# Performance work log

Hardware: AMD Instinct MI355X
Metric: run time of the kernel (lower is better)

## Reference

```python
import jax, jax.numpy as jnp
import numpy as np

C = 512
GROUPS = 8
EPS = 1e-5


def setup_inputs() -> dict:
    key = jax.random.key(0)
    ks = jax.random.split(key, 7)
    b, c, h, w = 32, C, 32, 32
    x = jax.random.normal(ks[0], (b, c, h, w), dtype=jnp.float32)
    norm_gamma = jnp.ones((c,), dtype=jnp.float32)
    norm_beta = jnp.zeros((c,), dtype=jnp.float32)
    # 1x1 convs == per-pixel linear layers; store as [out, in] matrices
    qkv_w = jax.random.normal(ks[1], (3 * c, c), dtype=jnp.float32) * (1.0 / np.sqrt(c))
    qkv_b = jnp.zeros((3 * c,), dtype=jnp.float32)
    out_w = jax.random.normal(ks[2], (c, c), dtype=jnp.float32) * (1.0 / np.sqrt(c))
    out_b = jnp.zeros((c,), dtype=jnp.float32)
    return {"x": x, "norm_gamma": norm_gamma, "norm_beta": norm_beta,
            "qkv_w": qkv_w, "qkv_b": qkv_b, "out_w": out_w, "out_b": out_b}


def group_norm(x, gamma, beta):
    b, c, h, w = x.shape
    xg = x.reshape(b, GROUPS, c // GROUPS, h, w)
    mean = jnp.mean(xg, axis=(2, 3, 4), keepdims=True)
    var = jnp.var(xg, axis=(2, 3, 4), keepdims=True)
    xg = (xg - mean) * jax.lax.rsqrt(var + EPS)
    x = xg.reshape(b, c, h, w)
    return x * gamma[None, :, None, None] + beta[None, :, None, None]


def reference(x, norm_gamma, norm_beta, qkv_w, qkv_b, out_w, out_b):
    b, c, h, w = x.shape
    xn = group_norm(x, norm_gamma, norm_beta)
    # 1x1 conv: [b,c,h,w] -> [b,3c,h,w]
    qkv = jnp.einsum('oc,bchw->bohw', qkv_w, xn) + qkv_b[None, :, None, None]
    q, k, v = jnp.split(qkv.reshape(b, 3 * c, h * w), 3, axis=1)  # each [b,c,hw]
    scale = c ** (-0.5)
    attn = jnp.einsum('bci,bcj->bij', q, k) * scale  # [b, hw, hw]
    attn = jax.nn.softmax(attn, axis=-1)
    out = jnp.einsum('bij,bcj->bci', attn, v).reshape(b, c, h, w)
    out = jnp.einsum('oc,bchw->bohw', out_w, out) + out_b[None, :, None, None]
    return x + out
```

## Files before the change

kernel.cpp:

```cpp
#include <hip/hip_runtime.h>

#define HW 1024
#define CD 512

typedef __bf16 bf16x8 __attribute__((ext_vector_type(8)));
typedef float f32x4 __attribute__((ext_vector_type(4)));

__device__ __forceinline__ unsigned short f2bf(float f) {
    unsigned int u = __float_as_uint(f);
    u += 0x7fff + ((u >> 16) & 1);
    return (unsigned short)(u >> 16);
}
__device__ __forceinline__ float bf2f(unsigned short h) {
    return __uint_as_float((unsigned)h << 16);
}

#define AS1(p) ((__attribute__((address_space(1))) void*)(p))
#define AS3(p) ((__attribute__((address_space(3))) void*)(p))
#define GLD16(gp, lp) __builtin_amdgcn_global_load_lds(AS1(gp), AS3(lp), 16, 0, 0)

__global__ __launch_bounds__(256)
void gn_stats(const float* __restrict__ x, float* __restrict__ mean, float* __restrict__ rstd) {
    int bg = blockIdx.x;
    const float4* p4 = (const float4*)(x + (size_t)bg * 65536);
    int tid = threadIdx.x;
    float s = 0.f, ss = 0.f;
#pragma unroll 8
    for (int it = 0; it < 64; ++it) {
        float4 v = p4[tid + it * 256];
        s  += v.x + v.y + v.z + v.w;
        ss += v.x * v.x + v.y * v.y + v.z * v.z + v.w * v.w;
    }
#pragma unroll
    for (int d = 32; d > 0; d >>= 1) { s += __shfl_down(s, d); ss += __shfl_down(ss, d); }
    __shared__ float ls[4], lss[4];
    if ((tid & 63) == 0) { ls[tid >> 6] = s; lss[tid >> 6] = ss; }
    __syncthreads();
    if (tid == 0) {
        float S = ls[0] + ls[1] + ls[2] + ls[3];
        float SS = lss[0] + lss[1] + lss[2] + lss[3];
        float m = S * (1.f / 65536.f);
        float v = SS * (1.f / 65536.f) - m * m;
        mean[bg] = m;
        rstd[bg] = rsqrtf(v + 1e-5f);
    }
}

__global__ __launch_bounds__(256)
void gn_norm_t(const float* __restrict__ x, const float* __restrict__ mean, const float* __restrict__ rstd,
               const float* __restrict__ gamma, const float* __restrict__ beta,
               unsigned short* __restrict__ xnT) {
    __shared__ unsigned short tile[64][67];
    int i0 = blockIdx.x * 64, c0 = blockIdx.y * 64, b = blockIdx.z;
    float m = mean[b * 8 + blockIdx.y];
    float r = rstd[b * 8 + blockIdx.y];
    int tid = threadIdx.x;
    int tr = tid >> 4, tc = (tid & 15) * 4;
    const float* xb = x + ((size_t)b * CD + c0) * HW + i0;
#pragma unroll
    for (int p = 0; p < 4; ++p) {
        int c = tr + p * 16;
        float g = gamma[c0 + c] * r;
        float bb = beta[c0 + c] - m * g;
        float4 v = *(const float4*)(xb + (size_t)c * HW + tc);
        tile[c][tc + 0] = f2bf(v.x * g + bb);
        tile[c][tc + 1] = f2bf(v.y * g + bb);
        tile[c][tc + 2] = f2bf(v.z * g + bb);
        tile[c][tc + 3] = f2bf(v.w * g + bb);
    }
    __syncthreads();
    unsigned short* ob = xnT + ((size_t)b * HW + i0) * CD + c0;
#pragma unroll
    for (int p = 0; p < 4; ++p) {
        int ir = tr + p * 16;
        ushort4 u;
        u.x = tile[tc + 0][ir];
        u.y = tile[tc + 1][ir];
        u.z = tile[tc + 2][ir];
        u.w = tile[tc + 3][ir];
        *(ushort4*)(ob + (size_t)ir * CD + tc) = u;
    }
}

__global__ __launch_bounds__(256)
void tpose3_bf16(const float* __restrict__ qkv_w, unsigned short* __restrict__ dst0) {
    __shared__ unsigned short tile[64][67];
    const int zmap[3] = {0, 2, 1};
    const float* src = qkv_w + (size_t)blockIdx.z * CD * CD;
    unsigned short* dst = dst0 + (size_t)zmap[blockIdx.z] * CD * CD;
    int i0 = blockIdx.x * 64, c0 = blockIdx.y * 64;
    int tid = threadIdx.x;
    int tr = tid >> 4, tc = (tid & 15) * 4;
#pragma unroll
    for (int p = 0; p < 4; ++p) {
        int r = tr + p * 16;
        float4 v = *(const float4*)(src + (size_t)(i0 + r) * CD + c0 + tc);
        tile[r][tc + 0] = f2bf(v.x);
        tile[r][tc + 1] = f2bf(v.y);
        tile[r][tc + 2] = f2bf(v.z);
        tile[r][tc + 3] = f2bf(v.w);
    }
    __syncthreads();
#pragma unroll
    for (int p = 0; p < 4; ++p) {
        int ir = tr + p * 16;
        ushort4 u;
        u.x = tile[tc + 0][ir];
        u.y = tile[tc + 1][ir];
        u.z = tile[tc + 2][ir];
        u.w = tile[tc + 3][ir];
        *(ushort4*)(dst + (size_t)(c0 + ir) * CD + i0 + tc) = u;
    }
}

__global__ __launch_bounds__(256)
void cvt_bf16(const float* __restrict__ src, unsigned short* __restrict__ dst) {
    int i = blockIdx.x * 256 + threadIdx.x;
    float4 v = ((const float4*)src)[i];
    ushort4 u;
    u.x = f2bf(v.x); u.y = f2bf(v.y); u.z = f2bf(v.z); u.w = f2bf(v.w);
    ((ushort4*)dst)[i] = u;
}

__global__ __launch_bounds__(256)
void gvec_kernel(const float* __restrict__ wk, const float* __restrict__ bq,
                 float* __restrict__ g) {
    __shared__ float red[4][64];
    int d = blockIdx.x * 64 + (threadIdx.x & 63);
    int os = threadIdx.x >> 6;
    float acc = 0.f;
    for (int o = os * 128; o < os * 128 + 128; ++o)
        acc += wk[(size_t)o * CD + d] * bq[o];
    red[os][threadIdx.x & 63] = acc;
    __syncthreads();
    if (threadIdx.x < 64)
        g[blockIdx.x * 64 + threadIdx.x] = red[0][threadIdx.x] + red[1][threadIdx.x] +
                                           red[2][threadIdx.x] + red[3][threadIdx.x];
}

__global__ __launch_bounds__(256)
void bias2_kernel(const float* __restrict__ out_w, const float* __restrict__ bv,
                  float* __restrict__ bias2) {
    int wid = threadIdx.x >> 6, lane = threadIdx.x & 63;
    int o = blockIdx.x * 4 + wid;
    float acc = 0.f;
#pragma unroll
    for (int t = 0; t < 512; t += 64)
        acc += out_w[(size_t)o * CD + t + lane] * bv[t + lane];
#pragma unroll
    for (int d = 32; d > 0; d >>= 1) acc += __shfl_down(acc, d);
    if (lane == 0) bias2[o] = acc;
}

template<int EPI>
__global__ __launch_bounds__(256, 2)
void gemm_bt(const unsigned short* __restrict__ A, const unsigned short* __restrict__ B,
             void* __restrict__ Cv, const float* __restrict__ bias,
             int M, int N, int K, long long sA, long long sB, long long sC) {
    unsigned nx = gridDim.x, ny = gridDim.y;
    unsigned lin = blockIdx.x + nx * (blockIdx.y + ny * blockIdx.z);
    unsigned nwg = nx * ny * gridDim.z;
    unsigned work = (lin & 7) * (nwg >> 3) + (lin >> 3);
    unsigned bx = work % nx; work /= nx;
    unsigned by = work % ny;
    unsigned bz = work / ny;

    A += (size_t)bz * sA;
    B += (size_t)bz * sB;
    int m0 = by * 128, n0 = bx * 128;

    __shared__ unsigned short lA[2][128 * 64];
    __shared__ unsigned short lB[2][128 * 64];

    int tid = threadIdx.x;
    int lane = tid & 63;
    int wr = (tid >> 6) >> 1, wc = (tid >> 6) & 1;

    f32x4 acc[4][4] = {};

    int strow[4], stcol[4];
#pragma unroll
    for (int s = 0; s < 4; ++s) {
        int row = (s * 256 + tid) >> 3;
        int g = (tid & 7) ^ (row & 7);
        strow[s] = row;
        stcol[s] = g * 8;
    }

    auto stage = [&](int buf, int k0) {
#pragma unroll
        for (int s = 0; s < 4; ++s) {
            GLD16(A + (size_t)(m0 + strow[s]) * K + k0 + stcol[s], &lA[buf][(size_t)(s * 256 + tid) * 8]);
            GLD16(B + (size_t)(n0 + strow[s]) * K + k0 + stcol[s], &lB[buf][(size_t)(s * 256 + tid) * 8]);
        }
    };

    int NT = K >> 6;
    stage(0, 0);
    __syncthreads();
    int cur = 0;
    for (int t = 0; t < NT; ++t) {
        if (t + 1 < NT) stage(cur ^ 1, (t + 1) << 6);
        const char* pa = (const char*)lA[cur];
        const char* pb = (const char*)lB[cur];
#pragma unroll
        for (int kk = 0; kk < 64; kk += 32) {
            bf16x8 af[4], bfr[4];
#pragma unroll
            for (int m = 0; m < 4; ++m) {
                int row = wr * 64 + m * 16 + (lane & 15);
                int off = (row * 128 + (kk + (lane >> 4) * 8) * 2) ^ ((row & 7) << 4);
                af[m] = *(const bf16x8*)(pa + off);
            }
#pragma unroll
            for (int n = 0; n < 4; ++n) {
                int row = wc * 64 + n * 16 + (lane & 15);
                int off = (row * 128 + (kk + (lane >> 4) * 8) * 2) ^ ((row & 7) << 4);
                bfr[n] = *(const bf16x8*)(pb + off);
            }
#pragma unroll
            for (int m = 0; m < 4; ++m)
#pragma unroll
                for (int n = 0; n < 4; ++n)
                    acc[m][n] = __builtin_amdgcn_mfma_f32_16x16x32_bf16(af[m], bfr[n], acc[m][n], 0, 0, 0);
        }
        __syncthreads();
        cur ^= 1;
    }

    int rl = (lane >> 4) * 4;
    int cl = lane & 15;
    unsigned short* Cb = (unsigned short*)Cv + (size_t)bz * sC;
#pragma unroll
    for (int m = 0; m < 4; ++m)
#pragma unroll
        for (int n = 0; n < 4; ++n) {
            int gm = m0 + wr * 64 + m * 16 + rl;
            int gn = n0 + wc * 64 + n * 16 + cl;
#pragma unroll
            for (int rg = 0; rg < 4; ++rg) {
                float v = acc[m][n][rg];
                if (EPI == 0) v += bias[gn];
                if (EPI == 1) v += bias[gm + rg];
                Cb[(size_t)(gm + rg) * N + gn] = f2bf(v);
            }
        }
}

__global__ __launch_bounds__(256, 2)
void scores_gemm(const unsigned short* __restrict__ T1, const unsigned short* __restrict__ xnT,
                 unsigned short* __restrict__ S, float* __restrict__ tmax, float* __restrict__ tsum) {
    unsigned nx = gridDim.x, ny = gridDim.y;
    unsigned lin = blockIdx.x + nx * (blockIdx.y + ny * blockIdx.z);
    unsigned nwg = nx * ny * gridDim.z;
    unsigned work = (lin & 7) * (nwg >> 3) + (lin >> 3);
    unsigned bx = work % nx; work /= nx;
    unsigned by = work % ny;
    unsigned bz = work / ny;

    const unsigned short* Ab = T1 + (size_t)bz * HW * CD;
    const unsigned short* Bb = xnT + (size_t)bz * HW * CD;
    int m0 = by * 128, n0 = bx * 128;

    __shared__ unsigned short lA[2][128 * 64];
    __shared__ unsigned short lB[2][128 * 64];
    __shared__ float redm[2][128];
    __shared__ float reds[2][128];

    int tid = threadIdx.x, lane = tid & 63;
    int wr = (tid >> 6) >> 1, wc = (tid >> 6) & 1;

    f32x4 acc[4][4] = {};
    int strow[4], stcol[4];
#pragma unroll
    for (int s = 0; s < 4; ++s) {
        int row = (s * 256 + tid) >> 3;
        int g = (tid & 7) ^ (row & 7);
        strow[s] = row;
        stcol[s] = g * 8;
    }

    auto stage = [&](int buf, int k0) {
#pragma unroll
        for (int s = 0; s < 4; ++s) {
            GLD16(Ab + (size_t)(m0 + strow[s]) * CD + k0 + stcol[s], &lA[buf][(size_t)(s * 256 + tid) * 8]);
            GLD16(Bb + (size_t)(n0 + strow[s]) * CD + k0 + stcol[s], &lB[buf][(size_t)(s * 256 + tid) * 8]);
        }
    };

    stage(0, 0);
    __syncthreads();
    int cur = 0;
    for (int t = 0; t < 8; ++t) {
        if (t < 7) stage(cur ^ 1, (t + 1) << 6);
        const char* pa = (const char*)lA[cur];
        const char* pb = (const char*)lB[cur];
#pragma unroll
        for (int kk = 0; kk < 64; kk += 32) {
            bf16x8 af[4], bfr[4];
#pragma unroll
            for (int m = 0; m < 4; ++m) {
                int row = wr * 64 + m * 16 + (lane & 15);
                int off = (row * 128 + (kk + (lane >> 4) * 8) * 2) ^ ((row & 7) << 4);
                af[m] = *(const bf16x8*)(pa + off);
            }
#pragma unroll
            for (int n = 0; n < 4; ++n) {
                int row = wc * 64 + n * 16 + (lane & 15);
                int off = (row * 128 + (kk + (lane >> 4) * 8) * 2) ^ ((row & 7) << 4);
                bfr[n] = *(const bf16x8*)(pb + off);
            }
#pragma unroll
            for (int m = 0; m < 4; ++m)
#pragma unroll
                for (int n = 0; n < 4; ++n)
                    acc[m][n] = __builtin_amdgcn_mfma_f32_16x16x32_bf16(af[m], bfr[n], acc[m][n], 0, 0, 0);
        }
        __syncthreads();
        cur ^= 1;
    }

    const float SL2E = 0.044194173824159216f * 1.4426950408889634f;
#pragma unroll
    for (int m = 0; m < 4; ++m)
#pragma unroll
        for (int n = 0; n < 4; ++n) acc[m][n] *= SL2E;

    int rl = (lane >> 4) * 4;
    int cl = lane & 15;

    float mr[4][4];
#pragma unroll
    for (int m = 0; m < 4; ++m)
#pragma unroll
        for (int rg = 0; rg < 4; ++rg)
            mr[m][rg] = fmaxf(fmaxf(acc[m][0][rg], acc[m][1][rg]),
                              fmaxf(acc[m][2][rg], acc[m][3][rg]));
#pragma unroll
    for (int d = 1; d < 16; d <<= 1)
#pragma unroll
        for (int m = 0; m < 4; ++m)
#pragma unroll
            for (int rg = 0; rg < 4; ++rg) mr[m][rg] = fmaxf(mr[m][rg], __shfl_xor(mr[m][rg], d));
    if ((lane & 15) == 0)
#pragma unroll
        for (int m = 0; m < 4; ++m)
#pragma unroll
            for (int rg = 0; rg < 4; ++rg) redm[wc][wr * 64 + m * 16 + rl + rg] = mr[m][rg];
    __syncthreads();
    float Mt[4][4];
#pragma unroll
    for (int m = 0; m < 4; ++m)
#pragma unroll
        for (int rg = 0; rg < 4; ++rg) {
            int row = wr * 64 + m * 16 + rl + rg;
            Mt[m][rg] = fmaxf(redm[0][row], redm[1][row]);
        }

    float sr[4][4] = {};
#pragma unroll
    for (int m = 0; m < 4; ++m)
#pragma unroll
        for (int n = 0; n < 4; ++n)
#pragma unroll
            for (int rg = 0; rg < 4; ++rg) {
                float e = __builtin_amdgcn_exp2f(acc[m][n][rg] - Mt[m][rg]);
                acc[m][n][rg] = e;
                sr[m][rg] += e;
            }
#pragma unroll
    for (int d = 1; d < 16; d <<= 1)
#pragma unroll
        for (int m = 0; m < 4; ++m)
#pragma unroll
            for (int rg = 0; rg < 4; ++rg) sr[m][rg] += __shfl_xor(sr[m][rg], d);
    if ((lane & 15) == 0)
#pragma unroll
        for (int m = 0; m < 4; ++m)
#pragma unroll
            for (int rg = 0; rg < 4; ++rg) reds[wc][wr * 64 + m * 16 + rl + rg] = sr[m][rg];
    __syncthreads();

    if (tid < 128) {
        float M = fmaxf(redm[0][tid], redm[1][tid]);
        float Z = reds[0][tid] + reds[1][tid];
        size_t o = ((size_t)bz * 8 + bx) * HW + m0 + tid;
        tmax[o] = M;
        tsum[o] = Z;
    }

    unsigned short* Sb = S + (size_t)bz * HW * HW;
#pragma unroll
    for (int m = 0; m < 4; ++m)
#pragma unroll
        for (int n = 0; n < 4; ++n) {
            int gm = m0 + wr * 64 + m * 16 + rl;
            int gn = n0 + wc * 64 + n * 16 + cl;
#pragma unroll
            for (int rg = 0; rg < 4; ++rg)
                Sb[(size_t)(gm + rg) * HW + gn] = f2bf(acc[m][n][rg]);
        }
}

__global__ __launch_bounds__(256)
void rescale_kernel(const float* __restrict__ tmax, const float* __restrict__ tsum,
                    float* __restrict__ ratio) {
    int r = blockIdx.x * 256 + threadIdx.x;
    int b = r >> 10, i = r & 1023;
    const float* tm = tmax + (size_t)b * 8 * HW + i;
    const float* ts = tsum + (size_t)b * 8 * HW + i;
    float M = -1e30f;
#pragma unroll
    for (int jt = 0; jt < 8; ++jt) M = fmaxf(M, tm[(size_t)jt * HW]);
    float Z = 0.f;
#pragma unroll
    for (int jt = 0; jt < 8; ++jt) Z += ts[(size_t)jt * HW] * __builtin_amdgcn_exp2f(tm[(size_t)jt * HW] - M);
    float rZ = 1.0f / Z;
#pragma unroll
    for (int jt = 0; jt < 7; ++jt)
        ratio[((size_t)b * 8 + jt) * HW + i] =
            __builtin_amdgcn_exp2f(tm[(size_t)jt * HW] - tm[(size_t)(jt + 1) * HW]);
    ratio[((size_t)b * 8 + 7) * HW + i] = __builtin_amdgcn_exp2f(tm[(size_t)7 * HW] - M) * rZ;
}

__global__ __launch_bounds__(256)
void pv_gemm(const unsigned short* __restrict__ A, const unsigned short* __restrict__ B,
             float* __restrict__ C, const float* __restrict__ bias,
             const float* __restrict__ resid, const float* __restrict__ ratio) {
    unsigned nx = gridDim.x, ny = gridDim.y;
    unsigned lin = blockIdx.x + nx * (blockIdx.y + ny * blockIdx.z);
    unsigned nwg = nx * ny * gridDim.z;
    unsigned work = (lin & 7) * (nwg >> 3) + (lin >> 3);
    unsigned bx = work % nx; work /= nx;
    unsigned by = work % ny;
    unsigned bz = work / ny;

    A += (size_t)bz * 512 * 1024;
    B += (size_t)bz * 1024 * 1024;
    int m0 = by * 128, n0 = bx * 128;

    __shared__ unsigned short lA[2][128 * 64];
    __shared__ unsigned short lB[2][128 * 64];

    int tid = threadIdx.x, lane = tid & 63;
    int wr = (tid >> 6) >> 1, wc = (tid >> 6) & 1;
    int cl = lane & 15;

    f32x4 acc[4][4] = {};

    int strow[4], stcol[4];
#pragma unroll
    for (int s = 0; s < 4; ++s) {
        int row = (s * 256 + tid) >> 3;
        int g = (tid & 7) ^ (row & 7);
        strow[s] = row;
        stcol[s] = g * 8;
    }

    auto stage = [&](int buf, int k0) {
#pragma unroll
        for (int s = 0; s < 4; ++s) {
            GLD16(A + (size_t)(m0 + strow[s]) * 1024 + k0 + stcol[s], &lA[buf][(size_t)(s * 256 + tid) * 8]);
            GLD16(B + (size_t)(n0 + strow[s]) * 1024 + k0 + stcol[s], &lB[buf][(size_t)(s * 256 + tid) * 8]);
        }
    };

    const float* rbase = ratio + (size_t)bz * 8 * HW + n0 + wc * 64 + cl;

    stage(0, 0);
    __syncthreads();
    int cur = 0;
    float r0 = 0.f, r1 = 0.f, r2 = 0.f, r3 = 0.f;
    for (int t = 0; t < 16; ++t) {
        if (t + 1 < 16) stage(cur ^ 1, (t + 1) << 6);
        if (!(t & 1)) {
            int jt = t >> 1;
            r0 = rbase[(size_t)jt * HW + 0];
            r1 = rbase[(size_t)jt * HW + 16];
            r2 = rbase[(size_t)jt * HW + 32];
            r3 = rbase[(size_t)jt * HW + 48];
        }
        const char* pa = (const char*)lA[cur];
        const char* pb = (const char*)lB[cur];
#pragma unroll
        for (int kk = 0; kk < 64; kk += 32) {
            bf16x8 af[4], bfr[4];
#pragma unroll
            for (int m = 0; m < 4; ++m) {
                int row = wr * 64 + m * 16 + (lane & 15);
                int off = (row * 128 + (kk + (lane >> 4) * 8) * 2) ^ ((row & 7) << 4);
                af[m] = *(const bf16x8*)(pa + off);
            }
#pragma unroll
            for (int n = 0; n < 4; ++n) {
                int row = wc * 64 + n * 16 + (lane & 15);
                int off = (row * 128 + (kk + (lane >> 4) * 8) * 2) ^ ((row & 7) << 4);
                bfr[n] = *(const bf16x8*)(pb + off);
            }
#pragma unroll
            for (int m = 0; m < 4; ++m)
#pragma unroll
                for (int n = 0; n < 4; ++n)
                    acc[m][n] = __builtin_amdgcn_mfma_f32_16x16x32_bf16(af[m], bfr[n], acc[m][n], 0, 0, 0);
        }
        __syncthreads();
        cur ^= 1;
        if (t & 1) {
#pragma unroll
            for (int m = 0; m < 4; ++m) {
                acc[m][0] *= r0;
                acc[m][1] *= r1;
                acc[m][2] *= r2;
                acc[m][3] *= r3;
            }
        }
    }

    int rl = (lane >> 4) * 4;
    float* Cf = C + (size_t)bz * 512 * 1024;
    const float* Rs = resid + (size_t)bz * 512 * 1024;
#pragma unroll
    for (int m = 0; m < 4; ++m)
#pragma unroll
        for (int n = 0; n < 4; ++n) {
            int gm = m0 + wr * 64 + m * 16 + rl;
            int gn = n0 + wc * 64 + n * 16 + cl;
#pragma unroll
            for (int rg = 0; rg < 4; ++rg) {
                size_t off = (size_t)(gm + rg) * 1024 + gn;
                Cf[off] = acc[m][n][rg] + bias[gm + rg] + Rs[off];
            }
        }
}

extern "C" void kernel_launch(void* const* d_in, const int* in_sizes, int n_in,
                              void* d_out, int out_size, void* d_ws, size_t ws_size,
                              hipStream_t stream) {
    const float* x      = (const float*)d_in[0];
    const float* gamma  = (const float*)d_in[1];
    const float* beta   = (const float*)d_in[2];
    const float* qkv_w  = (const float*)d_in[3];
    const float* qkv_b  = (const float*)d_in[4];
    const float* out_w  = (const float*)d_in[5];
    const float* out_b  = (const float*)d_in[6];

    char* ws = (char*)d_ws;
    unsigned short* xnT  = (unsigned short*)ws;
    unsigned short* vpr  = (unsigned short*)(ws + 33554432);
    unsigned short* SP   = (unsigned short*)(ws + 67108864);
    unsigned short* wqkT = (unsigned short*)(ws + 100663296);
    unsigned short* w2   = (unsigned short*)(ws + 101187584);
    float* gvec          = (float*)(ws + 101711872);
    float* bias2         = (float*)(ws + 101713920);
    float* meanp         = (float*)(ws + 101715968);
    float* rstdp         = (float*)(ws + 101716992);
    float* tmaxp         = (float*)(ws + 101718016);
    float* tsump         = (float*)(ws + 102766592);
    float* ratiop        = (float*)(ws + 103815168);

    unsigned short* slot0 = SP;
    unsigned short* owb   = SP + 786432;

    unsigned short* T1 = (unsigned short*)((char*)d_out + 33554432);
    float* outF = (float*)d_out;

    const float* wk_f = qkv_w + (size_t)512 * CD;

    gn_stats<<<256, 256, 0, stream>>>(x, meanp, rstdp);
    gn_norm_t<<<dim3(16, 8, 32), 256, 0, stream>>>(x, meanp, rstdp, gamma, beta, xnT);

    tpose3_bf16<<<dim3(8, 8, 3), 256, 0, stream>>>(qkv_w, slot0);
    cvt_bf16<<<256, 256, 0, stream>>>(out_w, owb);
    gvec_kernel<<<8, 256, 0, stream>>>(wk_f, qkv_b, gvec);
    bias2_kernel<<<128, 256, 0, stream>>>(out_w, qkv_b + 1024, bias2);

    gemm_bt<3><<<dim3(4, 4, 2), 256, 0, stream>>>(slot0 + 524288, slot0, wqkT, nullptr,
        512, 512, 512, 262144, 262144, 262144);

    gemm_bt<0><<<dim3(4, 8, 32), 256, 0, stream>>>(xnT, wqkT, T1, gvec,
        1024, 512, 512, 1024LL * 512, 0, 1024LL * 512);
    gemm_bt<1><<<dim3(8, 4, 32), 256, 0, stream>>>(w2, xnT, vpr, bias2,
        512, 1024, 512, 0, 1024LL * 512, 512LL * 1024);

    for (int h = 0; h < 2; ++h) {
        const unsigned short* T1h = T1 + (size_t)h * 16 * 1024 * 512;
        const unsigned short* xh  = xnT + (size_t)h * 16 * 1024 * 512;
        float* tmaxh = tmaxp + (size_t)h * 16 * 8 * 1024;
        float* tsumh = tsump + (size_t)h * 16 * 8 * 1024;

        scores_gemm<<<dim3(8, 8, 16), 256, 0, stream>>>(T1h, xh, SP, tmaxh, tsumh);
        rescale_kernel<<<64, 256, 0, stream>>>(tmaxh, tsumh, ratiop);
        pv_gemm<<<dim3(8, 4, 16), 256, 0, stream>>>(
            vpr + (size_t)h * 16 * 512 * 1024, SP,
            outF + (size_t)h * 16 * 512 * 1024, out_b,
            x + (size_t)h * 16 * 512 * 1024, ratiop);
    }
    (void)in_sizes; (void)n_in; (void)out_size; (void)ws_size;
}
```

Measured before the change: 222.9 us.

## Add 256x256-tile 8-wave GEMM kernel for the T1 and V projection GEMMs

New measurement: 220.6 us. No clear change (-1.0%).

```diff
diff --git a/kernel.cpp b/kernel.cpp
--- a/kernel.cpp
+++ b/kernel.cpp
@@ -18,6 +18,8 @@
 #define AS1(p) ((__attribute__((address_space(1))) void*)(p))
 #define AS3(p) ((__attribute__((address_space(3))) void*)(p))
 #define GLD16(gp, lp) __builtin_amdgcn_global_load_lds(AS1(gp), AS3(lp), 16, 0, 0)
+#define WAITVM(n) do { asm volatile("s_waitcnt vmcnt(" #n ")" ::: "memory"); \
+                       __builtin_amdgcn_sched_barrier(0); } while (0)
 
 __global__ __launch_bounds__(256)
 void gn_stats(const float* __restrict__ x, float* __restrict__ mean, float* __restrict__ rstd) {
@@ -150,6 +152,103 @@
 #pragma unroll
     for (int d = 32; d > 0; d >>= 1) acc += __shfl_down(acc, d);
     if (lane == 0) bias2[o] = acc;
+}
+
+template<int EPI>
+__global__ __launch_bounds__(512, 2)
+void gemm8(const unsigned short* __restrict__ A, const unsigned short* __restrict__ B,
+           unsigned short* __restrict__ C, const float* __restrict__ bias,
+           int M, int N, int K, long long sA, long long sB, long long sC) {
+    unsigned nx = gridDim.x, ny = gridDim.y;
+    unsigned lin = blockIdx.x + nx * (blockIdx.y + ny * blockIdx.z);
+    unsigned nwg = nx * ny * gridDim.z;
+    unsigned work = (lin & 7) * (nwg >> 3) + (lin >> 3);
+    unsigned bx = work % nx; work /= nx;
+    unsigned by = work % ny;
+    unsigned bz = work / ny;
+
+    A += (size_t)bz * sA;
+    B += (size_t)bz * sB;
+    int m0 = by * 256, n0 = bx * 256;
+
+    __shared__ unsigned short lA[2][256 * 64];
+    __shared__ unsigned short lB[2][256 * 64];
+
+    int tid = threadIdx.x, lane = tid & 63, wid = tid >> 6;
+    int wr = wid >> 2, wc = wid & 3;
+
+    f32x4 acc[8][4] = {};
+
+    int strow[4], stcol[4];
+#pragma unroll
+    for (int s = 0; s < 4; ++s) {
+        int idx = s * 512 + tid;
+        strow[s] = idx >> 3;
+        stcol[s] = ((idx & 7) ^ (strow[s] & 7)) * 8;
+    }
+
+    auto stage = [&](int buf, int kt) {
+        int k0 = kt << 6;
+#pragma unroll
+        for (int s = 0; s < 4; ++s)
+            GLD16(A + (size_t)(m0 + strow[s]) * K + k0 + stcol[s], &lA[buf][(size_t)(s * 512 + tid) * 8]);
+#pragma unroll
+        for (int s = 0; s < 4; ++s)
+            GLD16(B + (size_t)(n0 + strow[s]) * K + k0 + stcol[s], &lB[buf][(size_t)(s * 512 + tid) * 8]);
+    };
+
+    int NT = K >> 6;
+    stage(0, 0);
+    if (NT > 1) stage(1, 1);
+
+    for (int t = 0; t < NT; ++t) {
+        if (t < NT - 1) WAITVM(8); else WAITVM(0);
+        __builtin_amdgcn_s_barrier();
+        const char* pa = (const char*)lA[t & 1];
+        const char* pb = (const char*)lB[t & 1];
+        __builtin_amdgcn_s_setprio(1);
+#pragma unroll
+        for (int kk = 0; kk < 64; kk += 32) {
+            int koff = (kk + (lane >> 4) * 8) * 2;
+            bf16x8 af[8], bfr[4];
+#pragma unroll
+            for (int m = 0; m < 8; ++m) {
+                int row = wr * 128 + m * 16 + (lane & 15);
+                af[m] = *(const bf16x8*)(pa + ((row * 128 + koff) ^ ((row & 7) << 4)));
+            }
+#pragma unroll
+            for (int n = 0; n < 4; ++n) {
+                int row = wc * 64 + n * 16 + (lane & 15);
+                bfr[n] = *(const bf16x8*)(pb + ((row * 128 + koff) ^ ((row & 7) << 4)));
+            }
+#pragma unroll
+            for (int m = 0; m < 8; ++m)
+#pragma unroll
+                for (int n = 0; n < 4; ++n)
+                    acc[m][n] = __builtin_amdgcn_mfma_f32_16x16x32_bf16(af[m], bfr[n], acc[m][n], 0, 0, 0);
+        }
+        __builtin_amdgcn_s_setprio(0);
+        __builtin_amdgcn_s_barrier();
+        if (t + 2 < NT) stage(t & 1, t + 2);
+    }
+
+    int rl = (lane >> 4) * 4;
+    int cl = lane & 15;
+    unsigned short* Cb = C + (size_t)bz * sC;
+#pragma unroll
+    for (int m = 0; m < 8; ++m)
+#pragma unroll
+        for (int n = 0; n < 4; ++n) {
+            int gm = m0 + wr * 128 + m * 16 + rl;
+            int gn = n0 + wc * 64 + n * 16 + cl;
+#pragma unroll
+            for (int rg = 0; rg < 4; ++rg) {
+                float v = acc[m][n][rg];
+                if (EPI == 0) v += bias[gn];
+                if (EPI == 1) v += bias[gm + rg];
+                Cb[(size_t)(gm + rg) * N + gn] = f2bf(v);
+            }
+        }
 }
 
 template<int EPI>
@@ -577,9 +676,9 @@
     gemm_bt<3><<<dim3(4, 4, 2), 256, 0, stream>>>(slot0 + 524288, slot0, wqkT, nullptr,
         512, 512, 512, 262144, 262144, 262144);
 
-    gemm_bt<0><<<dim3(4, 8, 32), 256, 0, stream>>>(xnT, wqkT, T1, gvec,
+    gemm8<0><<<dim3(2, 4, 32), 512, 0, stream>>>(xnT, wqkT, T1, gvec,
         1024, 512, 512, 1024LL * 512, 0, 1024LL * 512);
-    gemm_bt<1><<<dim3(8, 4, 32), 256, 0, stream>>>(w2, xnT, vpr, bias2,
+    gemm8<1><<<dim3(4, 2, 32), 512, 0, stream>>>(w2, xnT, vpr, bias2,
         512, 1024, 512, 0, 1024LL * 512, 512LL * 1024);
 
     for (int h = 0; h < 2; ++h) {
```
